# Optimization experiments

Hardware: AMD Instinct MI355X
Metric: run time of the kernel (lower is better)

## Reference

```python
import jax, jax.numpy as jnp
import numpy as np

N = 50000      # nodes
E = 800000     # edges
FEAT = 128     # node_feat_size
HID = 128      # hidden_channels
LAT = 64       # latent_size
G = 256        # number of graphs in the batch


def _glorot_like(key, fan_in, shape):
    s = 1.0 / np.sqrt(fan_in)
    return jax.random.uniform(key, shape, jnp.float32, -s, s)


def setup_inputs() -> dict:
    key = jax.random.key(0)
    ks = jax.random.split(key, 13)
    x = jax.random.normal(ks[0], (N, FEAT), jnp.float32)
    edge_index = jax.random.randint(ks[1], (2, E), 0, N, dtype=jnp.int64)
    batch = jnp.sort(jax.random.randint(ks[2], (N,), 0, G, dtype=jnp.int64))
    return {
        "x": x,
        "edge_index": edge_index,
        "batch": batch,
        # GCNConv1: FEAT -> HID
        "W1": _glorot_like(ks[3], FEAT, (FEAT, HID)), "b1": jnp.zeros((HID,), jnp.float32),
        # GCNConv2: HID -> HID
        "W2": _glorot_like(ks[4], HID, (HID, HID)), "b2": jnp.zeros((HID,), jnp.float32),
        # fc: HID -> LAT
        "fcW": _glorot_like(ks[5], HID, (HID, LAT)), "fcb": _glorot_like(ks[6], HID, (LAT,)),
        # decoder: LAT -> HID
        "decW": _glorot_like(ks[7], LAT, (LAT, HID)), "decb": _glorot_like(ks[8], LAT, (HID,)),
        # GCNConv3: HID -> FEAT
        "W3": _glorot_like(ks[9], HID, (HID, FEAT)), "b3": jnp.zeros((FEAT,), jnp.float32),
    }


def reference(x, edge_index, batch, W1, b1, W2, b2, fcW, fcb, decW, decb, W3, b3):
    # --- GCN normalization with self-loops (computed once, shared by all convs) ---
    loop = jnp.arange(N, dtype=edge_index.dtype)
    row = jnp.concatenate([edge_index[0], loop])   # source nodes [E+N]
    col = jnp.concatenate([edge_index[1], loop])   # target nodes [E+N]
    deg = jax.ops.segment_sum(jnp.ones(row.shape, x.dtype), col, num_segments=N)
    dinv = jnp.where(deg > 0, jax.lax.rsqrt(deg), jnp.zeros_like(deg))
    norm = dinv[row] * dinv[col]                   # [E+N]

    def gcn(h, W, b):
        h = h @ W                                   # [N, out] transform first (PyG order)
        msg = h[row] * norm[:, None]                # gather + scale, [E+N, out]
        out = jax.ops.segment_sum(msg, col, num_segments=N)  # scatter-add
        return out + b

    # --- encode ---
    h = jax.nn.relu(gcn(x, W1, b1))
    h = jax.nn.relu(gcn(h, W2, b2))
    pooled = jax.ops.segment_sum(h, batch, num_segments=G)   # global_add_pool [G, HID]
    latent = jax.nn.relu(pooled @ fcW + fcb)                 # [G, LAT]

    # --- decode ---
    z = jax.nn.relu(latent @ decW + decb)                    # [G, HID]
    z = z[batch]                                             # broadcast back to nodes [N, HID]
    recon = gcn(z, W3, b3)                                   # [N, FEAT]
    return recon, latent
```

## Files before the change

### kernel.cpp

```cpp
#include <hip/hip_runtime.h>
#include <hip/hip_fp16.h>

static constexpr int NN   = 50000;
static constexpr int EE   = 800000;
static constexpr int GG   = 256;
static constexpr int PCH  = 16;
static constexpr int BK   = 128;
static constexpr int NB   = (NN + BK - 1) / BK;
static constexpr int CAP  = 4096;
static constexpr int CH   = 2048;
static constexpr int ABLK = (EE + CH - 1) / CH;
static constexpr int PBBB = EE / 64;

typedef _Float16 f16;
typedef f16  f16x8 __attribute__((ext_vector_type(8)));
typedef float f32x4 __attribute__((ext_vector_type(4)));

__device__ __forceinline__ int lowerb(const int* __restrict__ b, int n, int v) {
    int lo = 0, hi = n;
    while (lo < hi) { int m = (lo + hi) >> 1; if (b[m] < v) lo = m + 1; else hi = m; }
    return lo;
}

__global__ __launch_bounds__(256) void prep_k(const float* __restrict__ W1,
                                              const float* __restrict__ W2,
                                              f16x8* __restrict__ whi1, f16x8* __restrict__ wlo1,
                                              f16x8* __restrict__ whi2, f16x8* __restrict__ wlo2,
                                              int* __restrict__ bcur,
                                              float* __restrict__ pooled)
{
    int blk = blockIdx.x, t = threadIdx.x;
    if (blk < 16) {
        const float* W = (blk < 8) ? W1 : W2;
        f16x8* wh = (blk < 8) ? whi1 : whi2;
        f16x8* wl = (blk < 8) ? wlo1 : wlo2;
        int tid = (blk & 7) * 256 + t;
        int m  = tid & 15;
        int kq = (tid >> 4) & 3;
        int ks = (tid >> 6) & 3;
        int nt = tid >> 8;
        int n  = nt * 16 + m;
        int k0 = ks * 32 + kq * 8;
        f16x8 h8, l8;
        #pragma unroll
        for (int u = 0; u < 8; u++) {
            float x = W[(size_t)(k0 + u) * 128 + n];
            f16 h = (f16)x;
            h8[u] = h;
            l8[u] = (f16)(x - (float)h);
        }
        wh[tid] = h8;
        wl[tid] = l8;
    } else if (blk == 16) {
        for (int b = t; b < NB; b += 256) bcur[b] = b * CAP;
    } else {
        float4* p = (float4*)pooled;
        for (int j = (blk - 17) * 256 + t; j < GG * 32; j += 512)
            p[j] = make_float4(0.f, 0.f, 0.f, 0.f);
    }
}

__global__ __launch_bounds__(512) void binA_k(const int* __restrict__ ei,
                                              int* __restrict__ bcur,
                                              int2* __restrict__ eraw)
{
    __shared__ int2  stage[CH];
    __shared__ short sbid[CH];
    __shared__ int   hist[NB], loff[NB], gbase[NB], lcur[NB];
    __shared__ int   sc[512];

    int tid = threadIdx.x;
    int e0 = blockIdx.x * CH;
    int n = EE - e0; if (n > CH) n = CH;

    for (int b = tid; b < NB; b += 512) hist[b] = 0;
    __syncthreads();

    int2 r[CH / 512];
    #pragma unroll
    for (int k = 0; k < CH / 512; k++) {
        int s = k * 512 + tid;
        if (s < n) {
            int src = ei[e0 + s];
            int dst = ei[EE + e0 + s];
            r[k] = make_int2(src, dst);
            atomicAdd(&hist[dst >> 7], 1);
        }
    }
    __syncthreads();
    int v = (tid < NB) ? hist[tid] : 0;
    sc[tid] = v;
    __syncthreads();
    #pragma unroll
    for (int off = 1; off < 512; off <<= 1) {
        int add = (tid >= off) ? sc[tid - off] : 0;
        __syncthreads();
        sc[tid] += add;
        __syncthreads();
    }
    if (tid < NB) { int ex = sc[tid] - v; loff[tid] = ex; lcur[tid] = ex; }
    __syncthreads();
    for (int b = tid; b < NB; b += 512)
        gbase[b] = atomicAdd(&bcur[b], hist[b]);
    __syncthreads();
    #pragma unroll
    for (int k = 0; k < CH / 512; k++) {
        int s = k * 512 + tid;
        if (s < n) {
            int b = r[k].y >> 7;
            int slot = atomicAdd(&lcur[b], 1);
            stage[slot] = r[k];
            sbid[slot]  = (short)b;
        }
    }
    __syncthreads();
    for (int s = tid; s < n; s += 512) {
        int b = sbid[s];
        eraw[(size_t)gbase[b] + (s - loff[b])] = stage[s];
    }
}

__global__ __launch_bounds__(512) void scanb2_k(const int* __restrict__ bcur,
                                                int* __restrict__ bbase,
                                                int* __restrict__ rowptr)
{
    __shared__ int s[512];
    int t = threadIdx.x;
    int v = (t < NB) ? (bcur[t] - t * CAP) : 0;
    s[t] = v;
    __syncthreads();
    #pragma unroll
    for (int off = 1; off < 512; off <<= 1) {
        int add = (t >= off) ? s[t - off] : 0;
        __syncthreads();
        s[t] += add;
        __syncthreads();
    }
    if (t < NB) bbase[t] = s[t] - v;
    if (t == 0) rowptr[NN] = EE;
}

__global__ __launch_bounds__(512) void binB_k(const int2* __restrict__ eraw,
                                              const int* __restrict__ bcur,
                                              const int* __restrict__ bbase,
                                              int* __restrict__ rowptr,
                                              float* __restrict__ dinv,
                                              int* __restrict__ ebuf)
{
    __shared__ int hist[BK], excl[BK], cur[BK];
    int b = blockIdx.x, tid = threadIdx.x;
    int t0 = b << 7;
    int lim = NN - t0; if (lim > BK) lim = BK;
    int tot  = bcur[b] - b * CAP;
    int base = bbase[b];
    const int2* er = eraw + (size_t)b * CAP;

    if (tid < BK) hist[tid] = 0;
    __syncthreads();
    for (int s = tid; s < tot; s += 512) atomicAdd(&hist[er[s].y & 127], 1);
    __syncthreads();
    if (tid < BK) excl[tid] = hist[tid];
    __syncthreads();
    #pragma unroll
    for (int off = 1; off < BK; off <<= 1) {
        int add = (tid >= off && tid < BK) ? excl[tid - off] : 0;
        __syncthreads();
        if (tid < BK) excl[tid] += add;
        __syncthreads();
    }
    if (tid < BK) {
        int ex = excl[tid] - hist[tid];
        cur[tid] = base + ex;
        if (tid < lim) {
            rowptr[t0 + tid] = base + ex;
            dinv[t0 + tid]   = rsqrtf((float)(hist[tid] + 1));
        }
    }
    __syncthreads();
    for (int s = tid; s < tot; s += 512) {
        int2 rec = er[s];
        int p = atomicAdd(&cur[rec.y & 127], 1);
        ebuf[p] = rec.x;
    }
}

__global__ __launch_bounds__(512) void gemm_mfma3_k(const float* __restrict__ in,
                                                    const f16x8* __restrict__ whi_f,
                                                    const f16x8* __restrict__ wlo_f,
                                                    const float* __restrict__ dinv,
                                                    __half* __restrict__ out,
                                                    int rows)
{
    __shared__ __align__(16) f16x8 sh[2048];
    int tid  = threadIdx.x;
    #pragma unroll
    for (int u = 0; u < 4; u++) sh[u * 512 + tid] = whi_f[u * 512 + tid];
    __syncthreads();

    int lane = tid & 63;
    int wv   = tid >> 6;
    int rB   = blockIdx.x * 128 + wv * 16;
    int m    = lane & 15;
    int kq   = lane >> 4;
    int r    = rB + m;
    int rr   = (r < rows) ? r : (rows - 1);

    f16x8 ahi[4], alo[4];
    const float* rp = in + (size_t)rr * 128 + kq * 8;
    #pragma unroll
    for (int ks = 0; ks < 4; ks++) {
        float4 p0 = *(const float4*)(rp + ks * 32);
        float4 p1 = *(const float4*)(rp + ks * 32 + 4);
        float xs[8] = {p0.x, p0.y, p0.z, p0.w, p1.x, p1.y, p1.z, p1.w};
        #pragma unroll
        for (int u = 0; u < 8; u++) {
            f16 h = (f16)xs[u];
            ahi[ks][u] = h;
            alo[ks][u] = (f16)(xs[u] - (float)h);
        }
    }

    f32x4 acc[8];
    #pragma unroll
    for (int n = 0; n < 8; n++) acc[n] = (f32x4){0.f, 0.f, 0.f, 0.f};

    #pragma unroll
    for (int nt = 0; nt < 8; nt++) {
        #pragma unroll
        for (int ks = 0; ks < 4; ks++) {
            int idx = ((nt * 4 + ks) * 4 + kq) * 16 + m;
            f16x8 bh = sh[idx];
            f16x8 bl = wlo_f[idx];
            acc[nt] = __builtin_amdgcn_mfma_f32_16x16x32_f16(ahi[ks], bh, acc[nt], 0, 0, 0);
            acc[nt] = __builtin_amdgcn_mfma_f32_16x16x32_f16(alo[ks], bh, acc[nt], 0, 0, 0);
            acc[nt] = __builtin_amdgcn_mfma_f32_16x16x32_f16(ahi[ks], bl, acc[nt], 0, 0, 0);
        }
    }

    int   orow[4];
    float dv[4];
    #pragma unroll
    for (int j = 0; j < 4; j++) {
        int gr = rB + kq * 4 + j;
        orow[j] = gr;
        dv[j]   = (gr < rows) ? dinv[gr] : 0.f;
    }
    #pragma unroll
    for (int nt = 0; nt < 8; nt++) {
        int c = nt * 16 + m;
        #pragma unroll
        for (int j = 0; j < 4; j++) {
            if (orow[j] < rows)
                out[(size_t)orow[j] * 128 + c] = __float2half(acc[nt][j] * dv[j]);
        }
    }
}

__global__ __launch_bounds__(512) void gemm_mfma2h_k(const __half* __restrict__ in,
                                                     const f16x8* __restrict__ whi_f,
                                                     const f16x8* __restrict__ wlo_f,
                                                     const float* __restrict__ dinv,
                                                     __half* __restrict__ out,
                                                     int rows)
{
    __shared__ __align__(16) f16x8 sh[2048];
    int tid  = threadIdx.x;
    #pragma unroll
    for (int u = 0; u < 4; u++) sh[u * 512 + tid] = whi_f[u * 512 + tid];
    __syncthreads();

    int lane = tid & 63;
    int wv   = tid >> 6;
    int rB   = blockIdx.x * 128 + wv * 16;
    int m    = lane & 15;
    int kq   = lane >> 4;
    int r    = rB + m;
    int rr   = (r < rows) ? r : (rows - 1);

    f16x8 ah[4];
    const f16* rp = (const f16*)in + (size_t)rr * 128 + kq * 8;
    #pragma unroll
    for (int ks = 0; ks < 4; ks++)
        ah[ks] = *(const f16x8*)(rp + ks * 32);

    f32x4 acc[8];
    #pragma unroll
    for (int n = 0; n < 8; n++) acc[n] = (f32x4){0.f, 0.f, 0.f, 0.f};

    #pragma unroll
    for (int nt = 0; nt < 8; nt++) {
        #pragma unroll
        for (int ks = 0; ks < 4; ks++) {
            int idx = ((nt * 4 + ks) * 4 + kq) * 16 + m;
            f16x8 bh = sh[idx];
            f16x8 bl = wlo_f[idx];
            acc[nt] = __builtin_amdgcn_mfma_f32_16x16x32_f16(ah[ks], bh, acc[nt], 0, 0, 0);
            acc[nt] = __builtin_amdgcn_mfma_f32_16x16x32_f16(ah[ks], bl, acc[nt], 0, 0, 0);
        }
    }

    int   orow[4];
    float dv[4];
    #pragma unroll
    for (int j = 0; j < 4; j++) {
        int gr = rB + kq * 4 + j;
        orow[j] = gr;
        dv[j]   = (gr < rows) ? dinv[gr] : 0.f;
    }
    #pragma unroll
    for (int nt = 0; nt < 8; nt++) {
        int c = nt * 16 + m;
        #pragma unroll
        for (int j = 0; j < 4; j++) {
            if (orow[j] < rows)
                out[(size_t)orow[j] * 128 + c] = __float2half(acc[nt][j] * dv[j]);
        }
    }
}

__device__ __forceinline__ float4 gat4h(const __half* __restrict__ t, int s, int q)
{
    uint2 v = *(const uint2*)(t + ((size_t)s << 7) + q * 4);
    __half2 a = __builtin_bit_cast(__half2, v.x);
    __half2 b = __builtin_bit_cast(__half2, v.y);
    float2 fa = __half22float2(a), fb = __half22float2(b);
    return make_float4(fa.x, fa.y, fb.x, fb.y);
}

#define AGG_BODY                                                                 \
    int e0 = __builtin_amdgcn_readfirstlane(rowptr[i]);                          \
    int e1 = __builtin_amdgcn_readfirstlane(rowptr[i + 1]);                      \
    int deg = e1 - e0;                                                           \
    int idxsafe = (deg > 0) ? (e0 + min(lane, deg - 1)) : 0;                     \
    int myidx = ebuf[idxsafe];                                                   \
    float a0 = 0.f, a1 = 0.f, a2 = 0.f, a3 = 0.f;                                \
    if (half == 0) {                                                             \
        float4 v = gat4h(t, i, q);                                               \
        a0 = v.x; a1 = v.y; a2 = v.z; a3 = v.w;                                  \
    }                                                                            \
    int v   = min(deg, 64);                                                      \
    int c16 = v & ~15;                                                           \
    for (int j = half * 8; j < c16; j += 16) {                                   \
        int s0 = __shfl(myidx, j + 0), s1 = __shfl(myidx, j + 1);                \
        int s2 = __shfl(myidx, j + 2), s3 = __shfl(myidx, j + 3);                \
        int s4 = __shfl(myidx, j + 4), s5 = __shfl(myidx, j + 5);                \
        int s6 = __shfl(myidx, j + 6), s7 = __shfl(myidx, j + 7);                \
        float4 w0 = gat4h(t, s0, q);                                             \
        float4 w1 = gat4h(t, s1, q);                                             \
        float4 w2 = gat4h(t, s2, q);                                             \
        float4 w3 = gat4h(t, s3, q);                                             \
        float4 w4 = gat4h(t, s4, q);                                             \
        float4 w5 = gat4h(t, s5, q);                                             \
        float4 w6 = gat4h(t, s6, q);                                             \
        float4 w7 = gat4h(t, s7, q);                                             \
        a0 += w0.x + w1.x + w2.x + w3.x + w4.x + w5.x + w6.x + w7.x;             \
        a1 += w0.y + w1.y + w2.y + w3.y + w4.y + w5.y + w6.y + w7.y;             \
        a2 += w0.z + w1.z + w2.z + w3.z + w4.z + w5.z + w6.z + w7.z;             \
        a3 += w0.w + w1.w + w2.w + w3.w + w4.w + w5.w + w6.w + w7.w;             \
    }                                                                            \
    if (v - c16 >= 8) {                                                          \
        int j = c16 + half * 4;                                                  \
        int s0 = __shfl(myidx, j + 0), s1 = __shfl(myidx, j + 1);                \
        int s2 = __shfl(myidx, j + 2), s3 = __shfl(myidx, j + 3);                \
        float4 w0 = gat4h(t, s0, q);                                             \
        float4 w1 = gat4h(t, s1, q);                                             \
        float4 w2 = gat4h(t, s2, q);                                             \
        float4 w3 = gat4h(t, s3, q);                                             \
        a0 += w0.x + w1.x + w2.x + w3.x;                                         \
        a1 += w0.y + w1.y + w2.y + w3.y;                                         \
        a2 += w0.z + w1.z + w2.z + w3.z;                                         \
        a3 += w0.w + w1.w + w2.w + w3.w;                                         \
    }                                                                            \
    int done = c16 + ((v - c16) & 8);                                            \
    for (int j = done + half; j < v; j += 2) {                                   \
        int s = __shfl(myidx, j);                                                \
        float4 w = gat4h(t, s, q);                                               \
        a0 += w.x; a1 += w.y; a2 += w.z; a3 += w.w;                              \
    }                                                                            \
    for (int e = e0 + 64 + half; e < e1; e += 2) {                               \
        float4 w = gat4h(t, ebuf[e], q);                                         \
        a0 += w.x; a1 += w.y; a2 += w.z; a3 += w.w;                              \
    }                                                                            \
    a0 += __shfl_xor(a0, 32);                                                    \
    a1 += __shfl_xor(a1, 32);                                                    \
    a2 += __shfl_xor(a2, 32);                                                    \
    a3 += __shfl_xor(a3, 32);

__global__ __launch_bounds__(64) void aggh_k(const __half* __restrict__ t,
                                             const int* __restrict__ rowptr,
                                             const int* __restrict__ ebuf,
                                             const float* __restrict__ dinv,
                                             const float* __restrict__ bias,
                                             __half* __restrict__ out,
                                             const int* __restrict__ batch,
                                             int2* __restrict__ ebuf2)
{
    int bid  = blockIdx.x;
    int lane = threadIdx.x;
    if (bid >= NN) {
        int e = (bid - NN) * 64 + lane;
        if (e < EE) {
            int src = ebuf[e];
            ebuf2[e] = make_int2(batch[src], __float_as_int(dinv[src]));
        }
        return;
    }
    int i    = bid;
    int half = lane >> 5;
    int q    = lane & 31;
    AGG_BODY
    if (half == 0) {
        float di = dinv[i];
        float4 b = *(const float4*)(bias + q * 4);
        float ox = fmaxf(di * a0 + b.x, 0.f);
        float oy = fmaxf(di * a1 + b.y, 0.f);
        float oz = fmaxf(di * a2 + b.z, 0.f);
        float ow = fmaxf(di * a3 + b.w, 0.f);
        __half2 h01 = __floats2half2_rn(ox, oy);
        __half2 h23 = __floats2half2_rn(oz, ow);
        uint2 u = make_uint2(__builtin_bit_cast(unsigned, h01),
                             __builtin_bit_cast(unsigned, h23));
        *(uint2*)(out + (size_t)i * 128 + q * 4) = u;
    }
}

__global__ __launch_bounds__(64) void agg_out_k(const float* __restrict__ zz,
                                                const int* __restrict__ batch,
                                                const int* __restrict__ rowptr,
                                                const int2* __restrict__ ebuf2,
                                                const float* __restrict__ dinv,
                                                const float* __restrict__ bias,
                                                float* __restrict__ out)
{
    int i    = blockIdx.x;
    int lane = threadIdx.x;
    int half = lane >> 5;
    int q    = lane & 31;
    float di = dinv[i];

    float a0 = 0.f, a1 = 0.f, a2 = 0.f, a3 = 0.f;
    if (half == 0) {
        float4 v = *(const float4*)(zz + ((size_t)batch[i] << 7) + q * 4);
        a0 = di * v.x; a1 = di * v.y; a2 = di * v.z; a3 = di * v.w;
    }

    int e0 = rowptr[i], e1 = rowptr[i + 1];
    int deg = e1 - e0;
    int full = deg & ~7;
    int ee = e0 + full;
    for (int e = e0 + half * 4; e < ee; e += 8) {
        int2 r0 = ebuf2[e],     r1 = ebuf2[e + 1];
        int2 r2 = ebuf2[e + 2], r3 = ebuf2[e + 3];
        float4 w0 = *(const float4*)(zz + ((size_t)r0.x << 7) + q * 4);
        float4 w1 = *(const float4*)(zz + ((size_t)r1.x << 7) + q * 4);
        float4 w2 = *(const float4*)(zz + ((size_t)r2.x << 7) + q * 4);
        float4 w3 = *(const float4*)(zz + ((size_t)r3.x << 7) + q * 4);
        float n0 = __int_as_float(r0.y), n1 = __int_as_float(r1.y);
        float n2 = __int_as_float(r2.y), n3 = __int_as_float(r3.y);
        a0 += n0 * w0.x + n1 * w1.x + n2 * w2.x + n3 * w3.x;
        a1 += n0 * w0.y + n1 * w1.y + n2 * w2.y + n3 * w3.y;
        a2 += n0 * w0.z + n1 * w1.z + n2 * w2.z + n3 * w3.z;
        a3 += n0 * w0.w + n1 * w1.w + n2 * w2.w + n3 * w3.w;
    }
    for (int e = ee + half; e < e1; e += 2) {
        int2 r = ebuf2[e];
        float nm = __int_as_float(r.y);
        float4 w = *(const float4*)(zz + ((size_t)r.x << 7) + q * 4);
        a0 += nm * w.x; a1 += nm * w.y; a2 += nm * w.z; a3 += nm * w.w;
    }
    a0 += __shfl_xor(a0, 32);
    a1 += __shfl_xor(a1, 32);
    a2 += __shfl_xor(a2, 32);
    a3 += __shfl_xor(a3, 32);

    if (half == 0) {
        float4 b = *(const float4*)(bias + q * 4);
        float4 o;
        o.x = di * a0 + b.x;
        o.y = di * a1 + b.y;
        o.z = di * a2 + b.z;
        o.w = di * a3 + b.w;
        *(float4*)(out + (size_t)i * 128 + q * 4) = o;
    }
}

__global__ __launch_bounds__(128) void pool2_k(const __half* __restrict__ h2,
                                               const int* __restrict__ batch,
                                               float* __restrict__ pooled)
{
    int g = blockIdx.x;
    int c = blockIdx.y;
    int f = threadIdx.x;
    int bs = lowerb(batch, NN, g);
    int be = lowerb(batch, NN, g + 1);
    int len = be - bs;
    int cs = bs + (int)(((long long)len * c) / PCH);
    int ce = bs + (int)(((long long)len * (c + 1)) / PCH);
    float a = 0.f;
    for (int i = cs; i < ce; i++) a += __half2float(h2[(size_t)i * 128 + f]);
    if (ce > cs) atomicAdd(&pooled[(size_t)g * 128 + f], a);
}

__global__ __launch_bounds__(128) void fcdec_k(const float* __restrict__ pooled,
                                               const float* __restrict__ fcW,
                                               const float* __restrict__ fcb,
                                               const float* __restrict__ decW,
                                               const float* __restrict__ decb,
                                               const float* __restrict__ W3,
                                               float* __restrict__ lat_out,
                                               float* __restrict__ zz)
{
    __shared__ float lat[64];
    __shared__ float zs[128];
    int g = blockIdx.x, c = threadIdx.x;
    if (c < 64) {
        const float* p = pooled + (size_t)g * 128;
        float a = fcb[c];
        #pragma unroll 8
        for (int k = 0; k < 128; k++) a = fmaf(p[k], fcW[(size_t)k * 64 + c], a);
        a = fmaxf(a, 0.f);
        lat[c] = a;
        lat_out[(size_t)g * 64 + c] = a;
    }
    __syncthreads();
    {
        float a = decb[c];
        #pragma unroll 8
        for (int k = 0; k < 64; k++) a = fmaf(lat[k], decW[(size_t)k * 128 + c], a);
        zs[c] = fmaxf(a, 0.f);
    }
    __syncthreads();
    float o = 0.f;
    #pragma unroll 8
    for (int k = 0; k < 128; k++) o = fmaf(zs[k], W3[(size_t)k * 128 + c], o);
    zz[(size_t)g * 128 + c] = o;
}

extern "C" void kernel_launch(void* const* d_in, const int* in_sizes, int n_in,
                              void* d_out, int out_size, void* d_ws, size_t ws_size,
                              hipStream_t stream)
{
    const float* x     = (const float*)d_in[0];
    const int*   ei    = (const int*)d_in[1];
    const int*   batch = (const int*)d_in[2];
    const float* W1  = (const float*)d_in[3];
    const float* b1  = (const float*)d_in[4];
    const float* W2  = (const float*)d_in[5];
    const float* b2  = (const float*)d_in[6];
    const float* fcW = (const float*)d_in[7];
    const float* fcb = (const float*)d_in[8];
    const float* decW= (const float*)d_in[9];
    const float* decb= (const float*)d_in[10];
    const float* W3  = (const float*)d_in[11];
    const float* b3  = (const float*)d_in[12];

    char* ws = (char*)d_ws;
    size_t off = 0;
    auto alloc = [&](size_t bytes) -> char* {
        char* p = ws + off;
        off = (off + bytes + 255) & ~(size_t)255;
        return p;
    };
    float* dinv     = (float*)alloc((size_t)NN * 4);
    int*   rowptr   = (int*)alloc((size_t)(NN + 1) * 4);
    int*   bcur     = (int*)alloc((size_t)NB * 4);
    int*   bbase    = (int*)alloc((size_t)NB * 4);
    int*   ebuf     = (int*)alloc((size_t)EE * 4);
    int2*  ebuf2    = (int2*)alloc((size_t)EE * 8);
    float* pooled   = (float*)alloc((size_t)GG * 128 * 4);
    float* zz       = (float*)alloc((size_t)GG * 128 * 4);
    f16x8* whi1     = (f16x8*)alloc(2048 * 16);
    f16x8* wlo1     = (f16x8*)alloc(2048 * 16);
    f16x8* whi2     = (f16x8*)alloc(2048 * 16);
    f16x8* wlo2     = (f16x8*)alloc(2048 * 16);
    __half* A       = (__half*)alloc((size_t)NN * 128 * 2);
    __half* B       = (__half*)alloc((size_t)NN * 128 * 2);
    int2*  eraw     = (int2*)alloc((size_t)NB * CAP * 8);

    float* recon_out = (float*)d_out;
    float* lat_out   = (float*)d_out + (size_t)NN * 128;

    prep_k<<<19, 256, 0, stream>>>(W1, W2, whi1, wlo1, whi2, wlo2, bcur, pooled);
    binA_k<<<ABLK, 512, 0, stream>>>(ei, bcur, eraw);
    scanb2_k<<<1, 512, 0, stream>>>(bcur, bbase, rowptr);
    binB_k<<<NB, 512, 0, stream>>>(eraw, bcur, bbase, rowptr, dinv, ebuf);

    int gblk = (NN + 127) / 128;
    gemm_mfma3_k<<<gblk, 512, 0, stream>>>(x, whi1, wlo1, dinv, A, NN);
    aggh_k<<<NN + PBBB, 64, 0, stream>>>(A, rowptr, ebuf, dinv, b1, B, batch, ebuf2);
    gemm_mfma2h_k<<<gblk, 512, 0, stream>>>(B, whi2, wlo2, dinv, A, NN);
    aggh_k<<<NN, 64, 0, stream>>>(A, rowptr, ebuf, dinv, b2, B, batch, ebuf2);
    pool2_k<<<dim3(GG, PCH), 128, 0, stream>>>(B, batch, pooled);
    fcdec_k<<<GG, 128, 0, stream>>>(pooled, fcW, fcb, decW, decb, W3, lat_out, zz);
    agg_out_k<<<NN, 64, 0, stream>>>(zz, batch, rowptr, ebuf2, dinv,
                                     b3, recon_out);
}
```

Baseline: 271.8 us.

## Fold bucket scan into binB and pack edge records into 32-bit

Removes the single-block scan kernel: each binB block now computes its own base offset by reducing the counts of all preceding buckets in shared memory, and the last block writes rowptr[NN]. Separately, the decoder edge records (graph id plus source dinv) are packed into one 32-bit word, with the graph id in the low 16 bits and dinv stored as fp16, halving ebuf2 traffic in the output aggregation. The costs are redundant per-block reduction work and reduced precision of the normalization weight in the final conv.

```diff
diff --git a/kernel.cpp b/kernel.cpp
--- a/kernel.cpp
+++ b/kernel.cpp
@@ -20,6 +20,14 @@
     int lo = 0, hi = n;
     while (lo < hi) { int m = (lo + hi) >> 1; if (b[m] < v) lo = m + 1; else hi = m; }
     return lo;
+}
+
+__device__ __forceinline__ int pack_rec(int bg, float w) {
+    __half h = __float2half(w);
+    return bg | ((int)__builtin_bit_cast(unsigned short, h) << 16);
+}
+__device__ __forceinline__ float rec_w(int rec) {
+    return __half2float(__builtin_bit_cast(__half, (unsigned short)((unsigned)rec >> 16)));
 }
 
 __global__ __launch_bounds__(256) void prep_k(const float* __restrict__ W1,
@@ -120,39 +128,29 @@
     }
 }
 
-__global__ __launch_bounds__(512) void scanb2_k(const int* __restrict__ bcur,
-                                                int* __restrict__ bbase,
-                                                int* __restrict__ rowptr)
-{
-    __shared__ int s[512];
-    int t = threadIdx.x;
-    int v = (t < NB) ? (bcur[t] - t * CAP) : 0;
-    s[t] = v;
-    __syncthreads();
-    #pragma unroll
-    for (int off = 1; off < 512; off <<= 1) {
-        int add = (t >= off) ? s[t - off] : 0;
-        __syncthreads();
-        s[t] += add;
-        __syncthreads();
-    }
-    if (t < NB) bbase[t] = s[t] - v;
-    if (t == 0) rowptr[NN] = EE;
-}
-
 __global__ __launch_bounds__(512) void binB_k(const int2* __restrict__ eraw,
                                               const int* __restrict__ bcur,
-                                              const int* __restrict__ bbase,
                                               int* __restrict__ rowptr,
                                               float* __restrict__ dinv,
                                               int* __restrict__ ebuf)
 {
     __shared__ int hist[BK], excl[BK], cur[BK];
+    __shared__ int red[512];
     int b = blockIdx.x, tid = threadIdx.x;
     int t0 = b << 7;
     int lim = NN - t0; if (lim > BK) lim = BK;
-    int tot  = bcur[b] - b * CAP;
-    int base = bbase[b];
+    int tot = bcur[b] - b * CAP;
+
+    red[tid] = (tid < b) ? (bcur[tid] - tid * CAP) : 0;
+    __syncthreads();
+    #pragma unroll
+    for (int off = 256; off > 0; off >>= 1) {
+        if (tid < off) red[tid] += red[tid + off];
+        __syncthreads();
+    }
+    int base = red[0];
+    __syncthreads();
+
     const int2* er = eraw + (size_t)b * CAP;
 
     if (tid < BK) hist[tid] = 0;
@@ -176,6 +174,7 @@
             dinv[t0 + tid]   = rsqrtf((float)(hist[tid] + 1));
         }
     }
+    if (b == NB - 1 && tid == 0) rowptr[NN] = EE;
     __syncthreads();
     for (int s = tid; s < tot; s += 512) {
         int2 rec = er[s];
@@ -393,7 +392,7 @@
                                              const float* __restrict__ bias,
                                              __half* __restrict__ out,
                                              const int* __restrict__ batch,
-                                             int2* __restrict__ ebuf2)
+                                             int* __restrict__ ebuf2)
 {
     int bid  = blockIdx.x;
     int lane = threadIdx.x;
@@ -401,7 +400,7 @@
         int e = (bid - NN) * 64 + lane;
         if (e < EE) {
             int src = ebuf[e];
-            ebuf2[e] = make_int2(batch[src], __float_as_int(dinv[src]));
+            ebuf2[e] = pack_rec(batch[src], dinv[src]);
         }
         return;
     }
@@ -427,7 +426,7 @@
 __global__ __launch_bounds__(64) void agg_out_k(const float* __restrict__ zz,
                                                 const int* __restrict__ batch,
                                                 const int* __restrict__ rowptr,
-                                                const int2* __restrict__ ebuf2,
+                                                const int* __restrict__ ebuf2,
                                                 const float* __restrict__ dinv,
                                                 const float* __restrict__ bias,
                                                 float* __restrict__ out)
@@ -449,23 +448,23 @@
     int full = deg & ~7;
     int ee = e0 + full;
     for (int e = e0 + half * 4; e < ee; e += 8) {
-        int2 r0 = ebuf2[e],     r1 = ebuf2[e + 1];
-        int2 r2 = ebuf2[e + 2], r3 = ebuf2[e + 3];
-        float4 w0 = *(const float4*)(zz + ((size_t)r0.x << 7) + q * 4);
-        float4 w1 = *(const float4*)(zz + ((size_t)r1.x << 7) + q * 4);
-        float4 w2 = *(const float4*)(zz + ((size_t)r2.x << 7) + q * 4);
-        float4 w3 = *(const float4*)(zz + ((size_t)r3.x << 7) + q * 4);
-        float n0 = __int_as_float(r0.y), n1 = __int_as_float(r1.y);
-        float n2 = __int_as_float(r2.y), n3 = __int_as_float(r3.y);
+        int r0 = ebuf2[e],     r1 = ebuf2[e + 1];
+        int r2 = ebuf2[e + 2], r3 = ebuf2[e + 3];
+        float4 w0 = *(const float4*)(zz + ((size_t)(r0 & 0xffff) << 7) + q * 4);
+        float4 w1 = *(const float4*)(zz + ((size_t)(r1 & 0xffff) << 7) + q * 4);
+        float4 w2 = *(const float4*)(zz + ((size_t)(r2 & 0xffff) << 7) + q * 4);
+        float4 w3 = *(const float4*)(zz + ((size_t)(r3 & 0xffff) << 7) + q * 4);
+        float n0 = rec_w(r0), n1 = rec_w(r1);
+        float n2 = rec_w(r2), n3 = rec_w(r3);
         a0 += n0 * w0.x + n1 * w1.x + n2 * w2.x + n3 * w3.x;
         a1 += n0 * w0.y + n1 * w1.y + n2 * w2.y + n3 * w3.y;
         a2 += n0 * w0.z + n1 * w1.z + n2 * w2.z + n3 * w3.z;
         a3 += n0 * w0.w + n1 * w1.w + n2 * w2.w + n3 * w3.w;
     }
     for (int e = ee + half; e < e1; e += 2) {
-        int2 r = ebuf2[e];
-        float nm = __int_as_float(r.y);
-        float4 w = *(const float4*)(zz + ((size_t)r.x << 7) + q * 4);
+        int r = ebuf2[e];
+        float nm = rec_w(r);
+        float4 w = *(const float4*)(zz + ((size_t)(r & 0xffff) << 7) + q * 4);
         a0 += nm * w.x; a1 += nm * w.y; a2 += nm * w.z; a3 += nm * w.w;
     }
     a0 += __shfl_xor(a0, 32);
@@ -564,9 +563,8 @@
     float* dinv     = (float*)alloc((size_t)NN * 4);
     int*   rowptr   = (int*)alloc((size_t)(NN + 1) * 4);
     int*   bcur     = (int*)alloc((size_t)NB * 4);
-    int*   bbase    = (int*)alloc((size_t)NB * 4);
     int*   ebuf     = (int*)alloc((size_t)EE * 4);
-    int2*  ebuf2    = (int2*)alloc((size_t)EE * 8);
+    int*   ebuf2    = (int*)alloc((size_t)EE * 4);
     float* pooled   = (float*)alloc((size_t)GG * 128 * 4);
     float* zz       = (float*)alloc((size_t)GG * 128 * 4);
     f16x8* whi1     = (f16x8*)alloc(2048 * 16);
@@ -582,8 +580,7 @@
 
     prep_k<<<19, 256, 0, stream>>>(W1, W2, whi1, wlo1, whi2, wlo2, bcur, pooled);
     binA_k<<<ABLK, 512, 0, stream>>>(ei, bcur, eraw);
-    scanb2_k<<<1, 512, 0, stream>>>(bcur, bbase, rowptr);
-    binB_k<<<NB, 512, 0, stream>>>(eraw, bcur, bbase, rowptr, dinv, ebuf);
+    binB_k<<<NB, 512, 0, stream>>>(eraw, bcur, rowptr, dinv, ebuf);
 
     int gblk = (NN + 127) / 128;
     gemm_mfma3_k<<<gblk, 512, 0, stream>>>(x, whi1, wlo1, dinv, A, NN);
```

Result: faster. 266.0 us (-2.1%).
